# Performance work log

Hardware: AMD Instinct MI355X
Metric: run time of the kernel (lower is better)

The kernel has to match this reference:

```python
import jax, jax.numpy as jnp
import numpy as np

WIN_H = WIN_W = 7
NUM_HEADS = 6
DIM = 192
HEAD_DIM = DIM // NUM_HEADS
NUM_WIN = 1024
B_ = 8192
N = WIN_H * WIN_W


def _relative_position_index(win_h, win_w):
    coords = np.stack(np.meshgrid(np.arange(win_h), np.arange(win_w), indexing='ij'))  # (2,h,w)
    flat = coords.reshape(2, -1)
    rel = flat[:, :, None] - flat[:, None, :]          # (2, N, N)
    rel = rel.transpose(1, 2, 0).astype(np.int32)      # (N, N, 2)
    rel[:, :, 0] += win_h - 1
    rel[:, :, 1] += win_w - 1
    rel[:, :, 0] *= 2 * win_w - 1
    return rel.sum(-1)                                 # (N, N) in [0, (2h-1)(2w-1))


def setup_inputs() -> dict:
    key = jax.random.key(0)
    ks = jax.random.split(key, 7)
    return {
        'x': jax.random.normal(ks[0], (B_, N, DIM), jnp.float32),
        'mask': jax.random.normal(ks[1], (NUM_WIN, N, N), jnp.float32),
        'qkv_w': jax.random.normal(ks[2], (3 * DIM, DIM), jnp.float32) * 0.02,
        'qkv_b': jax.random.normal(ks[3], (3 * DIM,), jnp.float32) * 0.02,
        'proj_w': jax.random.normal(ks[4], (DIM, DIM), jnp.float32) * 0.02,
        'proj_b': jax.random.normal(ks[5], (DIM,), jnp.float32) * 0.02,
        'rpb_table': jax.random.normal(ks[6], ((2 * WIN_H - 1) * (2 * WIN_W - 1), NUM_HEADS), jnp.float32) * 0.02,
        'rel_index': jnp.asarray(_relative_position_index(WIN_H, WIN_W)),
    }


def reference(x, mask, qkv_w, qkv_b, proj_w, proj_b, rpb_table, rel_index):
    B, n, C = x.shape
    H, hd = NUM_HEADS, HEAD_DIM
    scale = hd ** (-0.5)

    qkv = (x @ qkv_w.T + qkv_b).reshape(B, n, 3, H, hd)
    qkv = jnp.transpose(qkv, (2, 0, 3, 1, 4))          # (3, B, H, N, hd)
    q, k, v = qkv[0], qkv[1], qkv[2]

    attn = jnp.einsum('bhnd,bhmd->bhnm', q * scale, k)  # (B, H, N, N)

    # gathered relative position bias: (N*N,) -> (N, N, H) -> (H, N, N)
    bias = rpb_table[rel_index.reshape(-1)].reshape(n, n, H)
    attn = attn + jnp.transpose(bias, (2, 0, 1))[None]

    num_win = mask.shape[0]
    attn = attn.reshape(B // num_win, num_win, H, n, n) + mask[None, :, None]
    attn = jax.nn.softmax(attn, axis=-1).reshape(B, H, n, n)

    out = jnp.einsum('bhnm,bhmd->bhnd', attn, v)         # (B, H, N, hd)
    out = jnp.transpose(out, (0, 2, 1, 3)).reshape(B, n, H * hd)
    return out @ proj_w.T + proj_b
```

## Files before the change

kernel.cpp:

```cpp
#include <hip/hip_runtime.h>

#define NTOK  49
#define NWIN  1024
#define SCALE 0.17677669529663687f

#define SMEM_BYTES 102400

typedef __bf16 bfx8 __attribute__((ext_vector_type(8)));
typedef float  f32x4 __attribute__((ext_vector_type(4)));
typedef unsigned long long ull;
typedef unsigned int uint;

union BF8 { bfx8 v; ull q[2]; };

__device__ __forceinline__ unsigned short f2bf(float f) {
    uint u = __builtin_bit_cast(uint, f);
    u += 0x7fffu + ((u >> 16) & 1u);
    return (unsigned short)(u >> 16);
}
__device__ __forceinline__ ull pack4(f32x4 a) {
    return (ull)f2bf(a[0]) | ((ull)f2bf(a[1]) << 16) |
           ((ull)f2bf(a[2]) << 32) | ((ull)f2bf(a[3]) << 48);
}
__device__ __forceinline__ f32x4 mfma16(bfx8 a, bfx8 b, f32x4 c) {
    return __builtin_amdgcn_mfma_f32_16x16x32_bf16(a, b, c, 0, 0, 0);
}

extern "C" __global__ void wattn_prep(const float* __restrict__ qkv_w,
                                      const float* __restrict__ proj_w,
                                      const float* __restrict__ rpb,
                                      const int*   __restrict__ rel,
                                      const float* __restrict__ qkv_b,
                                      unsigned short* __restrict__ W1f,
                                      unsigned short* __restrict__ W2p,
                                      float* __restrict__ qkvbs,
                                      float* __restrict__ biasN)
{
    const int i = blockIdx.x * 256 + threadIdx.x;
    if (i < 110592) {
        const int e = i & 7, l = (i >> 3) & 63, f = i >> 9;
        const int kk = f % 6, oct = f / 6;
        const int R = oct * 16 + (l & 15), C = kk * 32 + (l >> 4) * 8 + e;
        float v = qkv_w[R * 192 + C];
        if (oct < 12) v *= SCALE;
        W1f[i] = f2bf(v);
    }
    if (i < 36864) {
        const int e = i & 7, l = (i >> 3) & 63, f = i >> 9;
        const int c2t = f / 6, H = f % 6;
        const int R = c2t * 16 + (l & 15);
        const int C = H * 32 + (e >> 2) * 16 + (l >> 4) * 4 + (e & 3);
        W2p[i] = f2bf(proj_w[R * 192 + C]);
    }
    if (i < 576) qkvbs[i] = (i < 192) ? qkv_b[i] * SCALE : qkv_b[i];
    if (i < 6 * NTOK * 64) {
        const int h = i / (NTOK * 64), ii = (i / 64) % NTOK, j = i % 64;
        biasN[i] = (j < NTOK) ? rpb[rel[ii * NTOK + j] * 6 + h] : -1e30f;
    }
}

extern "C" __global__ void __launch_bounds__(512, 2)
wattn_fused(const float* __restrict__ x,
            const float* __restrict__ mask,
            const float* __restrict__ proj_b,
            const unsigned short* __restrict__ W1f,
            const unsigned short* __restrict__ W2p,
            const float* __restrict__ qkvbs,
            const float* __restrict__ biasN,
            float* __restrict__ out)
{
    __shared__ char smem[SMEM_BYTES];
    char* const XB  = smem;
    char* const OBX = smem;
    char* const QBp = smem + 25600;
    char* const KBp = smem + 50176;
    char* const VTp = smem + 74752;

    const int tid  = threadIdx.x;
    const int wave = tid >> 6;
    const int lane = tid & 63;
    const int g    = lane >> 4;
    const int jn   = lane & 15;
    const int qt   = wave & 3;
    const int hh   = wave >> 2;
    const size_t b = blockIdx.x;

#pragma unroll
    for (int u = 0; u < 3; ++u) {
        const int i = tid + u * 512;
        if (i < 1500)
            *(uint*)(XB + (49 + i / 100) * 400 + (i % 100) * 4) = 0u;
    }
    {
        const float4* xw = (const float4*)(x + b * 9408);
#pragma unroll
        for (int u = 0; u < 5; ++u) {
            const int i = tid + u * 512;
            if (i < 2352) {
                float4 v = xw[i];
                *(ull*)(XB + (i / 48) * 400 + (i % 48) * 8) =
                    (ull)f2bf(v.x) | ((ull)f2bf(v.y) << 16) |
                    ((ull)f2bf(v.z) << 32) | ((ull)f2bf(v.w) << 48);
            }
        }
    }
    __syncthreads();

#pragma unroll
    for (int jj = 0; jj < 2; ++jj) {
        const int pr = wave + 8 * jj;
        const int octA = pr * 2;
        bfx8 wfA[6], wfB[6];
#pragma unroll
        for (int kk = 0; kk < 6; ++kk) {
            wfA[kk] = *(const bfx8*)(W1f + ((size_t)(octA * 6 + kk) * 64 + lane) * 8);
            wfB[kk] = *(const bfx8*)(W1f + ((size_t)((octA + 1) * 6 + kk) * 64 + lane) * 8);
        }
        if (pr < 12) {
            const f32x4 biA = *(const f32x4*)(qkvbs + octA * 16 + 4 * g);
            const f32x4 biB = *(const f32x4*)(qkvbs + (octA + 1) * 16 + 4 * g);
            char* const dst = (pr < 6) ? QBp : KBp;
            const int pp = (pr < 6) ? pr : pr - 6;
#pragma unroll
            for (int tt = 0; tt < 4; ++tt) {
                f32x4 aA = biA, aB = biB;
#pragma unroll
                for (int kk = 0; kk < 6; ++kk) {
                    bfx8 xf = *(const bfx8*)(XB + (tt * 16 + jn) * 400 + kk * 64 + g * 16);
                    aA = mfma16(wfA[kk], xf, aA);
                    aB = mfma16(wfB[kk], xf, aB);
                }
                BF8 o; o.q[0] = pack4(aA); o.q[1] = pack4(aB);
                *(bfx8*)(dst + ((tt * 6 + pp) * 64 + lane) * 16) = o.v;
            }
        } else {
            const float bvA = qkvbs[octA * 16 + jn];
            const float bvB = qkvbs[(octA + 1) * 16 + jn];
            const int cA = octA - 24;
#pragma unroll
            for (int tt = 0; tt < 4; ++tt) {
                f32x4 aA = {bvA, bvA, bvA, bvA};
                f32x4 aB = {bvB, bvB, bvB, bvB};
#pragma unroll
                for (int kk = 0; kk < 6; ++kk) {
                    bfx8 xf = *(const bfx8*)(XB + (tt * 16 + jn) * 400 + kk * 64 + g * 16);
                    aA = mfma16(xf, wfA[kk], aA);
                    aB = mfma16(xf, wfB[kk], aB);
                }
                const int voff = (tt >> 1) * 64 + g * 16 + (tt & 1) * 8;
                *(ull*)(VTp + (cA * 16 + jn) * 144 + voff)       = pack4(aA);
                *(ull*)(VTp + ((cA + 1) * 16 + jn) * 144 + voff) = pack4(aB);
            }
        }
        __builtin_amdgcn_sched_barrier(0);
    }
    {
        const int octA = 32 + (wave >> 2) * 2;
        const int tt = wave & 3;
        bfx8 wfA[6], wfB[6];
#pragma unroll
        for (int kk = 0; kk < 6; ++kk) {
            wfA[kk] = *(const bfx8*)(W1f + ((size_t)(octA * 6 + kk) * 64 + lane) * 8);
            wfB[kk] = *(const bfx8*)(W1f + ((size_t)((octA + 1) * 6 + kk) * 64 + lane) * 8);
        }
        const float bvA = qkvbs[octA * 16 + jn];
        const float bvB = qkvbs[(octA + 1) * 16 + jn];
        f32x4 aA = {bvA, bvA, bvA, bvA};
        f32x4 aB = {bvB, bvB, bvB, bvB};
#pragma unroll
        for (int kk = 0; kk < 6; ++kk) {
            bfx8 xf = *(const bfx8*)(XB + (tt * 16 + jn) * 400 + kk * 64 + g * 16);
            aA = mfma16(xf, wfA[kk], aA);
            aB = mfma16(xf, wfB[kk], aB);
        }
        const int cA = octA - 24;
        const int voff = (tt >> 1) * 64 + g * 16 + (tt & 1) * 8;
        *(ull*)(VTp + (cA * 16 + jn) * 144 + voff)       = pack4(aA);
        *(ull*)(VTp + ((cA + 1) * 16 + jn) * 144 + voff) = pack4(aB);
    }
    __syncthreads();

    const int iq = qt * 16 + jn;
    const int ic = iq < NTOK ? iq : NTOK - 1;
    const float* mw = mask + (b & (NWIN - 1)) * (NTOK * NTOK);
    float mv[4][4];
#pragma unroll
    for (int kt = 0; kt < 4; ++kt)
#pragma unroll
        for (int r = 0; r < 4; ++r) {
            const int j = kt * 16 + 4 * g + r;
            const int jc = j < NTOK ? j : NTOK - 1;
            mv[kt][r] = mw[ic * NTOK + jc];
        }

#pragma unroll
    for (int hl = 0; hl < 3; ++hl) {
        const int H = hh * 3 + hl;
        bfx8 qfr = *(const bfx8*)(QBp + ((qt * 6 + H) * 64 + lane) * 16);
        f32x4 p[4];
#pragma unroll
        for (int kt = 0; kt < 4; ++kt) {
            bfx8 kf = *(const bfx8*)(KBp + ((kt * 6 + H) * 64 + lane) * 16);
            f32x4 z = {0.f, 0.f, 0.f, 0.f};
            p[kt] = mfma16(kf, qfr, z);
        }
        float mx = -1e30f;
#pragma unroll
        for (int kt = 0; kt < 4; ++kt) {
            const f32x4 bm4 = *(const f32x4*)(biasN + ((size_t)H * NTOK + ic) * 64 + kt * 16 + 4 * g);
#pragma unroll
            for (int r = 0; r < 4; ++r) {
                const float v = p[kt][r] + bm4[r] + mv[kt][r];
                p[kt][r] = v;
                mx = fmaxf(mx, v);
            }
        }
        mx = fmaxf(mx, __shfl_xor(mx, 16));
        mx = fmaxf(mx, __shfl_xor(mx, 32));
        float sum = 0.f;
#pragma unroll
        for (int kt = 0; kt < 4; ++kt)
#pragma unroll
            for (int r = 0; r < 4; ++r) {
                p[kt][r] = __expf(p[kt][r] - mx);
                sum += p[kt][r];
            }
        sum += __shfl_xor(sum, 16);
        sum += __shfl_xor(sum, 32);
        const float inv = 1.f / sum;
        BF8 p01, p23;
        p01.q[0] = pack4(p[0]); p01.q[1] = pack4(p[1]);
        p23.q[0] = pack4(p[2]); p23.q[1] = pack4(p[3]);
#pragma unroll
        for (int ct = 0; ct < 2; ++ct) {
            const int row = H * 32 + ct * 16 + jn;
            bfx8 v0 = *(const bfx8*)(VTp + row * 144 + g * 16);
            bfx8 v1 = *(const bfx8*)(VTp + row * 144 + 64 + g * 16);
            f32x4 o = {0.f, 0.f, 0.f, 0.f};
            o = mfma16(v0, p01.v, o);
            o = mfma16(v1, p23.v, o);
            *(ull*)(OBX + ((qt * 6 + H) * 64 + lane) * 16 + ct * 8) = pack4(o * inv);
        }
    }
    __syncthreads();

    float* outp = out + b * 9408;
#pragma unroll
    for (int t = 0; t < 3; ++t) {
        const int j = wave + 8 * t;
        const int c2t = j >> 1;
        const int qh  = j & 1;
        bfx8 wf2[6];
#pragma unroll
        for (int H = 0; H < 6; ++H)
            wf2[H] = *(const bfx8*)(W2p + ((size_t)(c2t * 6 + H) * 64 + lane) * 8);
        const f32x4 pb = *(const f32x4*)(proj_b + c2t * 16 + 4 * g);
#pragma unroll
        for (int t2 = 0; t2 < 2; ++t2) {
            const int qt2 = qh * 2 + t2;
            f32x4 acc = pb;
#pragma unroll
            for (int H = 0; H < 6; ++H) {
                bfx8 ob = *(const bfx8*)(OBX + ((qt2 * 6 + H) * 64 + lane) * 16);
                acc = mfma16(wf2[H], ob, acc);
            }
            const int tok = qt2 * 16 + jn;
            if (tok < NTOK)
                *(f32x4*)(outp + tok * 192 + c2t * 16 + 4 * g) = acc;
        }
    }
}

extern "C" void kernel_launch(void* const* d_in, const int* in_sizes, int n_in,
                              void* d_out, int out_size, void* d_ws, size_t ws_size,
                              hipStream_t stream) {
    const float* x      = (const float*)d_in[0];
    const float* mask   = (const float*)d_in[1];
    const float* qkv_w  = (const float*)d_in[2];
    const float* qkv_b  = (const float*)d_in[3];
    const float* proj_w = (const float*)d_in[4];
    const float* proj_b = (const float*)d_in[5];
    const float* rpb    = (const float*)d_in[6];
    const int*   rel    = (const int*)d_in[7];
    float* outp = (float*)d_out;

    char* ws = (char*)d_ws;
    unsigned short* W1f = (unsigned short*)ws;
    unsigned short* W2p = (unsigned short*)(ws + 221184);
    float* qkvbs        = (float*)(ws + 221184 + 73728);
    float* biasN        = (float*)(ws + 221184 + 73728 + 2304);

    wattn_prep<<<432, 256, 0, stream>>>(qkv_w, proj_w, rpb, rel, qkv_b,
                                        W1f, W2p, qkvbs, biasN);
    wattn_fused<<<8192, 512, 0, stream>>>(x, mask, proj_b,
                                          W1f, W2p, qkvbs, biasN, outp);
}
```

Measured before the change: 431.6 us.

## Shrink block to 4 waves, keep Q fragments in registers, drop Q smem

Halves the block to 256 threads (4 waves). Each wave now computes the Q projection for its own 16-token tile straight into registers, so the Q shared-memory buffer goes away and LDS per block drops from 100KB to 76KB. Each wave then runs all 6 heads for its query tile, and the K/V projection and output projection work is redistributed across 4 waves. The aim is more resident blocks per CU and less LDS traffic, at the cost of more serial work per wave and higher register pressure.

```diff
diff --git a/kernel.cpp b/kernel.cpp
--- a/kernel.cpp
+++ b/kernel.cpp
@@ -4,7 +4,7 @@
 #define NWIN  1024
 #define SCALE 0.17677669529663687f
 
-#define SMEM_BYTES 102400
+#define SMEM_BYTES 77824
 
 typedef __bf16 bfx8 __attribute__((ext_vector_type(8)));
 typedef float  f32x4 __attribute__((ext_vector_type(4)));
@@ -59,7 +59,7 @@
     }
 }
 
-extern "C" __global__ void __launch_bounds__(512, 2)
+extern "C" __global__ void __launch_bounds__(256, 2)
 wattn_fused(const float* __restrict__ x,
             const float* __restrict__ mask,
             const float* __restrict__ proj_b,
@@ -72,30 +72,28 @@
     __shared__ char smem[SMEM_BYTES];
     char* const XB  = smem;
     char* const OBX = smem;
-    char* const QBp = smem + 25600;
-    char* const KBp = smem + 50176;
-    char* const VTp = smem + 74752;
+    char* const KBp = smem + 25600;
+    char* const VTp = smem + 50176;
 
     const int tid  = threadIdx.x;
     const int wave = tid >> 6;
     const int lane = tid & 63;
     const int g    = lane >> 4;
     const int jn   = lane & 15;
-    const int qt   = wave & 3;
-    const int hh   = wave >> 2;
+    const int qt   = wave;
     const size_t b = blockIdx.x;
 
 #pragma unroll
-    for (int u = 0; u < 3; ++u) {
-        const int i = tid + u * 512;
+    for (int u = 0; u < 6; ++u) {
+        const int i = tid + u * 256;
         if (i < 1500)
             *(uint*)(XB + (49 + i / 100) * 400 + (i % 100) * 4) = 0u;
     }
     {
         const float4* xw = (const float4*)(x + b * 9408);
 #pragma unroll
-        for (int u = 0; u < 5; ++u) {
-            const int i = tid + u * 512;
+        for (int u = 0; u < 10; ++u) {
+            const int i = tid + u * 256;
             if (i < 2352) {
                 float4 v = xw[i];
                 *(ull*)(XB + (i / 48) * 400 + (i % 48) * 8) =
@@ -106,21 +104,47 @@
     }
     __syncthreads();
 
-#pragma unroll
-    for (int jj = 0; jj < 2; ++jj) {
-        const int pr = wave + 8 * jj;
-        const int octA = pr * 2;
+    BF8 qf6[6];
+    {
+        bfx8 xq[6];
+#pragma unroll
+        for (int kk = 0; kk < 6; ++kk)
+            xq[kk] = *(const bfx8*)(XB + (qt * 16 + jn) * 400 + kk * 64 + g * 16);
+#pragma unroll
+        for (int u = 0; u < 6; ++u) {
+            const int octA = 2 * u;
+            bfx8 wfA[6], wfB[6];
+#pragma unroll
+            for (int kk = 0; kk < 6; ++kk) {
+                wfA[kk] = *(const bfx8*)(W1f + ((size_t)(octA * 6 + kk) * 64 + lane) * 8);
+                wfB[kk] = *(const bfx8*)(W1f + ((size_t)((octA + 1) * 6 + kk) * 64 + lane) * 8);
+            }
+            f32x4 aA = *(const f32x4*)(qkvbs + octA * 16 + 4 * g);
+            f32x4 aB = *(const f32x4*)(qkvbs + (octA + 1) * 16 + 4 * g);
+#pragma unroll
+            for (int kk = 0; kk < 6; ++kk) {
+                aA = mfma16(wfA[kk], xq[kk], aA);
+                aB = mfma16(wfB[kk], xq[kk], aB);
+            }
+            qf6[u].q[0] = pack4(aA);
+            qf6[u].q[1] = pack4(aB);
+            __builtin_amdgcn_sched_barrier(0);
+        }
+    }
+
+#pragma unroll
+    for (int pp = 0; pp < 3; ++pp) {
+        const int p = wave + 4 * pp;
+        const int octA = 12 + 2 * p;
         bfx8 wfA[6], wfB[6];
 #pragma unroll
         for (int kk = 0; kk < 6; ++kk) {
             wfA[kk] = *(const bfx8*)(W1f + ((size_t)(octA * 6 + kk) * 64 + lane) * 8);
             wfB[kk] = *(const bfx8*)(W1f + ((size_t)((octA + 1) * 6 + kk) * 64 + lane) * 8);
         }
-        if (pr < 12) {
+        if (p < 6) {
             const f32x4 biA = *(const f32x4*)(qkvbs + octA * 16 + 4 * g);
             const f32x4 biB = *(const f32x4*)(qkvbs + (octA + 1) * 16 + 4 * g);
-            char* const dst = (pr < 6) ? QBp : KBp;
-            const int pp = (pr < 6) ? pr : pr - 6;
 #pragma unroll
             for (int tt = 0; tt < 4; ++tt) {
                 f32x4 aA = biA, aB = biB;
@@ -131,12 +155,12 @@
                     aB = mfma16(wfB[kk], xf, aB);
                 }
                 BF8 o; o.q[0] = pack4(aA); o.q[1] = pack4(aB);
-                *(bfx8*)(dst + ((tt * 6 + pp) * 64 + lane) * 16) = o.v;
+                *(bfx8*)(KBp + ((tt * 6 + p) * 64 + lane) * 16) = o.v;
             }
         } else {
             const float bvA = qkvbs[octA * 16 + jn];
             const float bvB = qkvbs[(octA + 1) * 16 + jn];
-            const int cA = octA - 24;
+            const int cA = 2 * p - 12;
 #pragma unroll
             for (int tt = 0; tt < 4; ++tt) {
                 f32x4 aA = {bvA, bvA, bvA, bvA};
@@ -154,30 +178,6 @@
         }
         __builtin_amdgcn_sched_barrier(0);
     }
-    {
-        const int octA = 32 + (wave >> 2) * 2;
-        const int tt = wave & 3;
-        bfx8 wfA[6], wfB[6];
-#pragma unroll
-        for (int kk = 0; kk < 6; ++kk) {
-            wfA[kk] = *(const bfx8*)(W1f + ((size_t)(octA * 6 + kk) * 64 + lane) * 8);
-            wfB[kk] = *(const bfx8*)(W1f + ((size_t)((octA + 1) * 6 + kk) * 64 + lane) * 8);
-        }
-        const float bvA = qkvbs[octA * 16 + jn];
-        const float bvB = qkvbs[(octA + 1) * 16 + jn];
-        f32x4 aA = {bvA, bvA, bvA, bvA};
-        f32x4 aB = {bvB, bvB, bvB, bvB};
-#pragma unroll
-        for (int kk = 0; kk < 6; ++kk) {
-            bfx8 xf = *(const bfx8*)(XB + (tt * 16 + jn) * 400 + kk * 64 + g * 16);
-            aA = mfma16(xf, wfA[kk], aA);
-            aB = mfma16(xf, wfB[kk], aB);
-        }
-        const int cA = octA - 24;
-        const int voff = (tt >> 1) * 64 + g * 16 + (tt & 1) * 8;
-        *(ull*)(VTp + (cA * 16 + jn) * 144 + voff)       = pack4(aA);
-        *(ull*)(VTp + ((cA + 1) * 16 + jn) * 144 + voff) = pack4(aB);
-    }
     __syncthreads();
 
     const int iq = qt * 16 + jn;
@@ -194,15 +194,13 @@
         }
 
 #pragma unroll
-    for (int hl = 0; hl < 3; ++hl) {
-        const int H = hh * 3 + hl;
-        bfx8 qfr = *(const bfx8*)(QBp + ((qt * 6 + H) * 64 + lane) * 16);
+    for (int H = 0; H < 6; ++H) {
         f32x4 p[4];
 #pragma unroll
         for (int kt = 0; kt < 4; ++kt) {
             bfx8 kf = *(const bfx8*)(KBp + ((kt * 6 + H) * 64 + lane) * 16);
             f32x4 z = {0.f, 0.f, 0.f, 0.f};
-            p[kt] = mfma16(kf, qfr, z);
+            p[kt] = mfma16(kf, qf6[H].v, z);
         }
         float mx = -1e30f;
 #pragma unroll
@@ -246,18 +244,15 @@
 
     float* outp = out + b * 9408;
 #pragma unroll
-    for (int t = 0; t < 3; ++t) {
-        const int j = wave + 8 * t;
-        const int c2t = j >> 1;
-        const int qh  = j & 1;
+    for (int u = 0; u < 3; ++u) {
+        const int c2t = wave * 3 + u;
         bfx8 wf2[6];
 #pragma unroll
         for (int H = 0; H < 6; ++H)
             wf2[H] = *(const bfx8*)(W2p + ((size_t)(c2t * 6 + H) * 64 + lane) * 8);
         const f32x4 pb = *(const f32x4*)(proj_b + c2t * 16 + 4 * g);
 #pragma unroll
-        for (int t2 = 0; t2 < 2; ++t2) {
-            const int qt2 = qh * 2 + t2;
+        for (int qt2 = 0; qt2 < 4; ++qt2) {
             f32x4 acc = pb;
 #pragma unroll
             for (int H = 0; H < 6; ++H) {
@@ -268,6 +263,7 @@
             if (tok < NTOK)
                 *(f32x4*)(outp + tok * 192 + c2t * 16 + 4 * g) = acc;
         }
+        __builtin_amdgcn_sched_barrier(0);
     }
 }
 
@@ -292,6 +288,6 @@
 
     wattn_prep<<<432, 256, 0, stream>>>(qkv_w, proj_w, rpb, rel, qkv_b,
                                         W1f, W2p, qkvbs, biasN);
-    wattn_fused<<<8192, 512, 0, stream>>>(x, mask, proj_b,
+    wattn_fused<<<8192, 256, 0, stream>>>(x, mask, proj_b,
                                           W1f, W2p, qkvbs, biasN, outp);
 }
```

Measured after the change: 448.1 us. 3.8% more time.
